# Performance work log

Hardware: AMD Instinct MI355X
Metric: run time of the kernel (lower is better)

The kernel has to match this reference:

```python
import jax, jax.numpy as jnp
import numpy as np

N_NODES = 100000
N_EDGES = 1600000
N_PAIRS = 200000
IN_C, HID_C, OUT_C = 128, 128, 64


def setup_inputs() -> dict:
    key = jax.random.key(0)
    ks = jax.random.split(key, 10)
    x = jax.random.normal(ks[0], (N_NODES, IN_C), dtype=jnp.float32)
    edge_index = jax.random.randint(ks[1], (2, N_EDGES), 0, N_NODES, dtype=jnp.int64)
    node_i = jax.random.randint(ks[2], (N_PAIRS,), 0, N_NODES, dtype=jnp.int64)
    node_j = jax.random.randint(ks[3], (N_PAIRS,), 0, N_NODES, dtype=jnp.int64)
    def glorot(k, fan_in, fan_out):
        s = jnp.sqrt(6.0 / (fan_in + fan_out))
        return jax.random.uniform(k, (fan_in, fan_out), jnp.float32, -s, s)
    W1 = glorot(ks[4], IN_C, HID_C)
    b1 = jnp.zeros((HID_C,), jnp.float32)
    W2 = glorot(ks[5], HID_C, HID_C)
    b2 = jnp.zeros((HID_C,), jnp.float32)
    W3 = glorot(ks[6], HID_C, OUT_C)
    b3 = jnp.zeros((OUT_C,), jnp.float32)
    return {"x": x, "edge_index": edge_index, "node_i": node_i, "node_j": node_j,
            "W1": W1, "b1": b1, "W2": W2, "b2": b2, "W3": W3, "b3": b3}


def _gcn_layer(h, src, dst, deg_inv, w_e, W, b):
    # h: [N, Cin] -> linear then symmetric-normalized aggregation (with self loops)
    h = h @ W  # [N, Cout]
    msg = h[src] * w_e[:, None]  # [E, Cout] gather + edge weight
    agg = jax.ops.segment_sum(msg, dst, num_segments=N_NODES)
    agg = agg + h * deg_inv[:, None]  # self-loop term: h_i / deg_i
    return agg + b


def reference(x, edge_index, node_i, node_j, W1, b1, W2, b2, W3, b3):
    src, dst = edge_index[0], edge_index[1]
    # GCN normalization with self loops: deg_i = 1 + in-degree
    ones = jnp.ones((N_EDGES,), jnp.float32)
    deg = jax.ops.segment_sum(ones, dst, num_segments=N_NODES) + 1.0
    dinv_sqrt = jax.lax.rsqrt(deg)
    deg_inv = 1.0 / deg
    w_e = dinv_sqrt[src] * dinv_sqrt[dst]  # [E]

    h = _gcn_layer(x, src, dst, deg_inv, w_e, W1, b1)
    h = jax.nn.relu(h)  # dropout is identity in eval mode
    h = _gcn_layer(h, src, dst, deg_inv, w_e, W2, b2)
    h = jax.nn.relu(h)
    h = _gcn_layer(h, src, dst, deg_inv, w_e, W3, b3)

    # dot-product link decode (decode_type=None)
    return jnp.sum(h[node_i] * h[node_j], axis=-1)  # [N_PAIRS]
```

## Files before the change

kernel.cpp:

```cpp
#include <hip/hip_runtime.h>

#define NN 100000
#define NNP 100032
#define NE 1600000
#define NP 200000
#define NBKT 782
#define BCAP 3072
#define BKB 4096

typedef short s16x8 __attribute__((ext_vector_type(8)));
typedef float f32x4 __attribute__((ext_vector_type(4)));
typedef float f32x2 __attribute__((ext_vector_type(2)));

__device__ __forceinline__ unsigned short f2bf(float f) {
  unsigned int u = __float_as_uint(f);
  u += 0x7fffu + ((u >> 16) & 1u);
  return (unsigned short)(u >> 16);
}

__device__ __forceinline__ void pkadd(f32x2& a, uint u) {
  f32x2 v;
  v.x = __uint_as_float(u << 16);
  v.y = __uint_as_float(u & 0xffff0000u);
  asm("v_pk_add_f32 %0, %0, %1" : "+v"(a) : "v"(v));
}

__device__ __forceinline__ void rowadd(uint4 v, f32x2* a) {
  pkadd(a[0], v.x);
  pkadd(a[1], v.y);
  pkadd(a[2], v.z);
  pkadd(a[3], v.w);
}

template <int RSH>
__device__ __forceinline__ void gath(const int* __restrict__ col,
                                     const char* __restrict__ Tb, int s,
                                     int tend, uint co, f32x2* acc) {
  const int d = tend - s;
  const int nfull = d >> 3;
  const int rem = d & 7;
  int e = s;
  int c[8];
#pragma unroll
  for (int j = 0; j < 8; ++j) c[j] = col[e + j];
#pragma unroll 1
  for (int it = 0; it < nfull; ++it) {
    uint4 v0 = *(const uint4*)(Tb + (((uint)c[0] << RSH) | co));
    uint4 v1 = *(const uint4*)(Tb + (((uint)c[1] << RSH) | co));
    uint4 v2 = *(const uint4*)(Tb + (((uint)c[2] << RSH) | co));
    uint4 v3 = *(const uint4*)(Tb + (((uint)c[3] << RSH) | co));
    uint4 v4 = *(const uint4*)(Tb + (((uint)c[4] << RSH) | co));
    uint4 v5 = *(const uint4*)(Tb + (((uint)c[5] << RSH) | co));
    uint4 v6 = *(const uint4*)(Tb + (((uint)c[6] << RSH) | co));
    uint4 v7 = *(const uint4*)(Tb + (((uint)c[7] << RSH) | co));
    e += 8;
#pragma unroll
    for (int j = 0; j < 8; ++j) c[j] = col[e + j];
    rowadd(v0, acc);
    rowadd(v1, acc);
    rowadd(v2, acc);
    rowadd(v3, acc);
    rowadd(v4, acc);
    rowadd(v5, acc);
    rowadd(v6, acc);
    rowadd(v7, acc);
  }
  if (rem) {
#pragma unroll
    for (int j = 0; j < 8; ++j) c[j] = (j < rem) ? c[j] : NN;
    uint4 v0 = *(const uint4*)(Tb + (((uint)c[0] << RSH) | co));
    uint4 v1 = *(const uint4*)(Tb + (((uint)c[1] << RSH) | co));
    uint4 v2 = *(const uint4*)(Tb + (((uint)c[2] << RSH) | co));
    uint4 v3 = *(const uint4*)(Tb + (((uint)c[3] << RSH) | co));
    uint4 v4 = *(const uint4*)(Tb + (((uint)c[4] << RSH) | co));
    uint4 v5 = *(const uint4*)(Tb + (((uint)c[5] << RSH) | co));
    uint4 v6 = *(const uint4*)(Tb + (((uint)c[6] << RSH) | co));
    uint4 v7 = *(const uint4*)(Tb + (((uint)c[7] << RSH) | co));
    rowadd(v0, acc);
    rowadd(v1, acc);
    rowadd(v2, acc);
    rowadd(v3, acc);
    rowadd(v4, acc);
    rowadd(v5, acc);
    rowadd(v6, acc);
    rowadd(v7, acc);
  }
}

template <int NT>
__device__ __forceinline__ void prepw_dev(const float* __restrict__ W,
                                          uint* __restrict__ Wt, int tid) {
  constexpr int COUT = NT * 16;
  if (tid >= 4 * NT * 64) return;
  int lane = tid & 63, comb = tid >> 6;
  int ks = comb / NT, tl = comb % NT;
  int q = lane >> 4, n = lane & 15;
  uint w[4];
#pragma unroll
  for (int jj = 0; jj < 4; ++jj) {
    int k0 = ks * 32 + q * 8 + 2 * jj;
    uint lo = f2bf(W[k0 * COUT + tl * 16 + n]);
    uint hi = f2bf(W[(k0 + 1) * COUT + tl * 16 + n]);
    w[jj] = lo | (hi << 16);
  }
  ((uint4*)Wt)[comb * 64 + lane] = make_uint4(w[0], w[1], w[2], w[3]);
}

__global__ __launch_bounds__(256) void k_setup(const float* __restrict__ W1,
                                               const float* __restrict__ W2,
                                               const float* __restrict__ W3,
                                               uint* __restrict__ Wt1,
                                               uint* __restrict__ Wt2,
                                               uint* __restrict__ Wt3,
                                               int* __restrict__ gcur) {
  int b = blockIdx.x, t = threadIdx.x;
  if (b < 4) {
    int i = b * 256 + t;
    if (i < 1024) gcur[i] = 0;
  } else if (b < 12) {
    prepw_dev<8>(W1, Wt1, (b - 4) * 256 + t);
  } else if (b < 20) {
    prepw_dev<8>(W2, Wt2, (b - 12) * 256 + t);
  } else {
    prepw_dev<4>(W3, Wt3, (b - 20) * 256 + t);
  }
}

__global__ __launch_bounds__(256) void k_bucket(const int* __restrict__ ei,
                                                int* __restrict__ gcur,
                                                int* __restrict__ aux) {
  __shared__ int cnt[1024];
  __shared__ int scn[1024];
  __shared__ int cur[1024];
  __shared__ int sc[256];
  __shared__ int sorted[BKB];
  __shared__ unsigned short sbkt[BKB];
  const int t = threadIdx.x;
  const int base = blockIdx.x * BKB;

  for (int i = t; i < 1024; i += 256) cnt[i] = 0;
  __syncthreads();

  int pk[16], bk[16];
#pragma unroll
  for (int i = 0; i < 16; ++i) {
    int e = base + t + 256 * i;
    if (e < NE) {
      int src = ei[e], dst = ei[NE + e];
      bk[i] = dst >> 7;
      pk[i] = src | ((dst & 127) << 17);
      atomicAdd(&cnt[bk[i]], 1);
    } else {
      bk[i] = -1;
    }
  }
  __syncthreads();

  int s0 = cnt[4 * t], s1 = cnt[4 * t + 1], s2 = cnt[4 * t + 2], s3 = cnt[4 * t + 3];
  int local = s0 + s1 + s2 + s3;
  sc[t] = local;
  __syncthreads();
  for (int off = 1; off < 256; off <<= 1) {
    int a = (t >= off) ? sc[t - off] : 0;
    __syncthreads();
    sc[t] += a;
    __syncthreads();
  }
  int b0 = sc[t] - local;
  scn[4 * t] = b0;
  scn[4 * t + 1] = b0 + s0;
  scn[4 * t + 2] = b0 + s0 + s1;
  scn[4 * t + 3] = b0 + s0 + s1 + s2;
  cur[4 * t] = scn[4 * t];
  cur[4 * t + 1] = scn[4 * t + 1];
  cur[4 * t + 2] = scn[4 * t + 2];
  cur[4 * t + 3] = scn[4 * t + 3];
  __syncthreads();
  const int tot = sc[255];

#pragma unroll
  for (int i = 0; i < 16; ++i) {
    if (bk[i] >= 0) {
      int pos = atomicAdd(&cur[bk[i]], 1);
      sorted[pos] = pk[i];
      sbkt[pos] = (unsigned short)bk[i];
    }
  }
  __syncthreads();

  for (int b = t; b < 1024; b += 256) {
    int c = cnt[b];
    if (c > 0) cur[b] = b * BCAP + atomicAdd(&gcur[b], c);
  }
  __syncthreads();

  for (int k = t; k < tot; k += 256) {
    int b = sbkt[k];
    aux[cur[b] + (k - scn[b])] = sorted[k];
  }
}

__global__ __launch_bounds__(256) void k_csr(const int* __restrict__ gcur,
                                             const int* __restrict__ aux,
                                             int* __restrict__ row_ptr,
                                             float* __restrict__ dinv,
                                             int* __restrict__ col) {
  __shared__ int red[256];
  __shared__ int c[128];
  __shared__ int cur[128];
  const int b = blockIdx.x, t = threadIdx.x;
  int p = 0;
  for (int i = t; i < b; i += 256) p += gcur[i];
  red[t] = p;
  if (t < 128) c[t] = 0;
  __syncthreads();
  for (int off = 128; off > 0; off >>= 1) {
    if (t < off) red[t] += red[t + off];
    __syncthreads();
  }
  const int base = red[0];
  const int m = gcur[b];
  const int* a = aux + (size_t)b * BCAP;
  __syncthreads();
  for (int k = t; k < m; k += 256) atomicAdd(&c[a[k] >> 17], 1);
  __syncthreads();
  int val = (t < 128) ? c[t] : 0;
  red[t] = val;
  __syncthreads();
  for (int off = 1; off < 128; off <<= 1) {
    int add = (t >= off && t < 128) ? red[t - off] : 0;
    __syncthreads();
    if (t < 128) red[t] += add;
    __syncthreads();
  }
  if (t < 128) {
    int excl = red[t] - val + base;
    int node = b * 128 + t;
    if (node < NN) {
      row_ptr[node] = excl;
      dinv[node] = rsqrtf((float)(val + 1));
      cur[t] = excl;
    }
  }
  if (b == NBKT - 1 && t == 0) row_ptr[NN] = base + m;
  __syncthreads();
  for (int k = t; k < m; k += 256) {
    int pk2 = a[k];
    int pos = atomicAdd(&cur[pk2 >> 17], 1);
    col[pos] = pk2 & 0x1FFFF;
  }
}

__global__ __launch_bounds__(256) void k_gemm1(const float* __restrict__ A,
                                               const uint* __restrict__ Wt,
                                               const float* __restrict__ dinv,
                                               unsigned short* __restrict__ T) {
  constexpr int NT = 8, COUT = 128;
  __shared__ __align__(16) uint Wlds[4 * NT * 64 * 4];
  __shared__ __align__(16) unsigned short Obuf[64 * COUT];
  const int t = threadIdx.x;
  {
    const uint4* src = (const uint4*)Wt;
    uint4* dst = (uint4*)Wlds;
    for (int i = t; i < 4 * NT * 64; i += 256) dst[i] = src[i];
  }
  __syncthreads();

  const int wv = t >> 6, lane = t & 63;
  const int n = lane & 15, quad = lane >> 4;
  const int rbase = blockIdx.x * 64 + wv * 16;

  union AB { uint4 u; s16x8 s; };
  AB a[4];
  {
    int row = rbase + n;
    if (row >= NN) row = NN - 1;
    const float* ap = A + (size_t)row * 128;
#pragma unroll
    for (int ks = 0; ks < 4; ++ks) {
      float4 v0 = *(const float4*)(ap + ks * 32 + quad * 8);
      float4 v1 = *(const float4*)(ap + ks * 32 + quad * 8 + 4);
      a[ks].u.x = (uint)f2bf(v0.x) | ((uint)f2bf(v0.y) << 16);
      a[ks].u.y = (uint)f2bf(v0.z) | ((uint)f2bf(v0.w) << 16);
      a[ks].u.z = (uint)f2bf(v1.x) | ((uint)f2bf(v1.y) << 16);
      a[ks].u.w = (uint)f2bf(v1.z) | ((uint)f2bf(v1.w) << 16);
    }
  }

  f32x4 acc[NT];
#pragma unroll
  for (int tl = 0; tl < NT; ++tl) acc[tl] = (f32x4){0.f, 0.f, 0.f, 0.f};

#pragma unroll
  for (int ks = 0; ks < 4; ++ks) {
#pragma unroll
    for (int tl = 0; tl < NT; ++tl) {
      AB b;
      b.u = *(const uint4*)&Wlds[((ks * NT + tl) * 64 + lane) * 4];
      acc[tl] = __builtin_amdgcn_mfma_f32_16x16x32_bf16(a[ks].s, b.s, acc[tl], 0, 0, 0);
    }
  }

  float4 dv = *(const float4*)(dinv + rbase + quad * 4);
  float dvv[4] = {dv.x, dv.y, dv.z, dv.w};
  unsigned short* ob = Obuf + wv * 16 * COUT;
#pragma unroll
  for (int tl = 0; tl < NT; ++tl)
#pragma unroll
    for (int r = 0; r < 4; ++r)
      ob[(quad * 4 + r) * COUT + tl * 16 + n] = f2bf(acc[tl][r] * dvv[r]);

  uint4* gdst = (uint4*)(T + (size_t)rbase * COUT);
#pragma unroll
  for (int i = 0; i < 4; ++i) {
    int off16 = i * 64 + lane;
    int lrow = (off16 * 8) / COUT;
    uint4 v = make_uint4(0u, 0u, 0u, 0u);
    if (rbase + lrow < NN) v = *(const uint4*)&ob[off16 * 8];
    gdst[off16] = v;
  }
}

template <int COUT>
__global__ __launch_bounds__(256) void k_gg(const int* __restrict__ row_ptr,
                                            const int* __restrict__ col,
                                            const uint4* __restrict__ T4,
                                            const float* __restrict__ dinv,
                                            const float* __restrict__ bias,
                                            const uint4* __restrict__ Wt,
                                            unsigned short* __restrict__ Tout) {
  constexpr int NT = COUT / 16;
  constexpr int TLW = NT / 4;
  constexpr int OSTR = COUT + 8;
  __shared__ __align__(16) uint4 Alds[16 * 17];
  const int t = threadIdx.x, wv = t >> 6, lane = t & 63;
  const int nbase = blockIdx.x * 16;
  const int q = lane >> 4, cl = lane & 15;

  const int node = nbase + wv * 4 + q;
  int s = 0, tend = 0;
  if (node < NN) {
    s = row_ptr[node];
    tend = row_ptr[node + 1];
  }
  const char* Tb = (const char*)T4;
  const uint co = (uint)cl << 4;
  f32x2 acc[4];
  acc[0] = (f32x2){0.f, 0.f};
  acc[1] = (f32x2){0.f, 0.f};
  acc[2] = (f32x2){0.f, 0.f};
  acc[3] = (f32x2){0.f, 0.f};
  rowadd(*(const uint4*)(Tb + (((uint)node << 8) | co)), acc);
  gath<8>(col, Tb, s, tend, co, acc);

  {
    float dv = dinv[node];
    float4 b0 = *(const float4*)&bias[cl * 8];
    float4 b1 = *(const float4*)&bias[cl * 8 + 4];
    float r0 = fmaxf(fmaf(dv, acc[0].x, b0.x), 0.f);
    float r1 = fmaxf(fmaf(dv, acc[0].y, b0.y), 0.f);
    float r2 = fmaxf(fmaf(dv, acc[1].x, b0.z), 0.f);
    float r3 = fmaxf(fmaf(dv, acc[1].y, b0.w), 0.f);
    float r4 = fmaxf(fmaf(dv, acc[2].x, b1.x), 0.f);
    float r5 = fmaxf(fmaf(dv, acc[2].y, b1.y), 0.f);
    float r6 = fmaxf(fmaf(dv, acc[3].x, b1.z), 0.f);
    float r7 = fmaxf(fmaf(dv, acc[3].y, b1.w), 0.f);
    uint4 o;
    o.x = (uint)f2bf(r0) | ((uint)f2bf(r1) << 16);
    o.y = (uint)f2bf(r2) | ((uint)f2bf(r3) << 16);
    o.z = (uint)f2bf(r4) | ((uint)f2bf(r5) << 16);
    o.w = (uint)f2bf(r6) | ((uint)f2bf(r7) << 16);
    Alds[(wv * 4 + q) * 17 + cl] = o;
  }
  __syncthreads();

  const int n = lane & 15, quad = lane >> 4;
  union AB { uint4 u; s16x8 s; };
  AB a[4];
#pragma unroll
  for (int ks = 0; ks < 4; ++ks) a[ks].u = Alds[n * 17 + ks * 4 + quad];
  f32x4 acc2[TLW];
#pragma unroll
  for (int j = 0; j < TLW; ++j) acc2[j] = (f32x4){0.f, 0.f, 0.f, 0.f};
#pragma unroll
  for (int ks = 0; ks < 4; ++ks) {
#pragma unroll
    for (int j = 0; j < TLW; ++j) {
      int tl = wv * TLW + j;
      AB b;
      b.u = Wt[(ks * NT + tl) * 64 + lane];
      acc2[j] = __builtin_amdgcn_mfma_f32_16x16x32_bf16(a[ks].s, b.s, acc2[j], 0, 0, 0);
    }
  }
  __syncthreads();

  unsigned short* Obuf = (unsigned short*)Alds;
  float4 dv4 = *(const float4*)(dinv + nbase + quad * 4);
  float dvv[4] = {dv4.x, dv4.y, dv4.z, dv4.w};
#pragma unroll
  for (int j = 0; j < TLW; ++j) {
    int tl = wv * TLW + j;
#pragma unroll
    for (int r = 0; r < 4; ++r)
      Obuf[(quad * 4 + r) * OSTR + tl * 16 + n] = f2bf(acc2[j][r] * dvv[r]);
  }
  __syncthreads();

  if constexpr (COUT == 128) {
    int row = t >> 4, c16 = t & 15;
    uint4 v = make_uint4(0u, 0u, 0u, 0u);
    if (nbase + row < NN) v = *(const uint4*)&Obuf[row * OSTR + c16 * 8];
    ((uint4*)(Tout + (size_t)nbase * COUT))[row * 16 + c16] = v;
  } else {
    if (t < 128) {
      int row = t >> 3, c16 = t & 7;
      uint4 v = make_uint4(0u, 0u, 0u, 0u);
      if (nbase + row < NN) v = *(const uint4*)&Obuf[row * OSTR + c16 * 8];
      ((uint4*)(Tout + (size_t)nbase * COUT))[row * 8 + c16] = v;
    }
  }
}

__global__ __launch_bounds__(256) void k_gather3(const int* __restrict__ row_ptr,
                                                 const int* __restrict__ col,
                                                 const uint4* __restrict__ T4,
                                                 uint4* __restrict__ G3) {
  const int wid = (blockIdx.x * 256 + threadIdx.x) >> 6;
  const int lane = threadIdx.x & 63;
  const int g = lane >> 3, cl = lane & 7;
  const int node = wid * 8 + g;
  if (node >= NN) return;
  int s = row_ptr[node], tend = row_ptr[node + 1];
  const char* Tb = (const char*)T4;
  const uint co = (uint)cl << 4;
  f32x2 acc[4];
  acc[0] = (f32x2){0.f, 0.f};
  acc[1] = (f32x2){0.f, 0.f};
  acc[2] = (f32x2){0.f, 0.f};
  acc[3] = (f32x2){0.f, 0.f};
  rowadd(*(const uint4*)(Tb + (((uint)node << 7) | co)), acc);
  gath<7>(col, Tb, s, tend, co, acc);
  uint4 o;
  o.x = (uint)f2bf(acc[0].x) | ((uint)f2bf(acc[0].y) << 16);
  o.y = (uint)f2bf(acc[1].x) | ((uint)f2bf(acc[1].y) << 16);
  o.z = (uint)f2bf(acc[2].x) | ((uint)f2bf(acc[2].y) << 16);
  o.w = (uint)f2bf(acc[3].x) | ((uint)f2bf(acc[3].y) << 16);
  G3[(size_t)node * 8 + cl] = o;
}

__global__ __launch_bounds__(256) void k_decode(const int* __restrict__ ni,
                                                const int* __restrict__ nj,
                                                const uint2* __restrict__ G3,
                                                const float* __restrict__ dinv,
                                                const float* __restrict__ b3,
                                                float* __restrict__ out) {
  int p = blockIdx.x * 16 + (threadIdx.x >> 4);
  int cl = threadIdx.x & 15;
  int i = ni[p], j = nj[p];
  uint2 ui = G3[(size_t)i * 16 + cl];
  uint2 uj = G3[(size_t)j * 16 + cl];
  float4 bb = *(const float4*)&b3[cl * 4];
  float di = dinv[i], dj = dinv[j];
  float gi0 = __uint_as_float(ui.x << 16), gi1 = __uint_as_float(ui.x & 0xffff0000u);
  float gi2 = __uint_as_float(ui.y << 16), gi3 = __uint_as_float(ui.y & 0xffff0000u);
  float gj0 = __uint_as_float(uj.x << 16), gj1 = __uint_as_float(uj.x & 0xffff0000u);
  float gj2 = __uint_as_float(uj.y << 16), gj3 = __uint_as_float(uj.y & 0xffff0000u);
  float v = fmaf(di, gi0, bb.x) * fmaf(dj, gj0, bb.x) +
            fmaf(di, gi1, bb.y) * fmaf(dj, gj1, bb.y) +
            fmaf(di, gi2, bb.z) * fmaf(dj, gj2, bb.z) +
            fmaf(di, gi3, bb.w) * fmaf(dj, gj3, bb.w);
  v += __shfl_xor(v, 1, 64);
  v += __shfl_xor(v, 2, 64);
  v += __shfl_xor(v, 4, 64);
  v += __shfl_xor(v, 8, 64);
  if (cl == 0) out[p] = v;
}

extern "C" void kernel_launch(void* const* d_in, const int* in_sizes, int n_in,
                              void* d_out, int out_size, void* d_ws, size_t ws_size,
                              hipStream_t stream) {
  const float* x  = (const float*)d_in[0];
  const int*   ei = (const int*)d_in[1];
  const int*   ni = (const int*)d_in[2];
  const int*   nj = (const int*)d_in[3];
  const float* W1 = (const float*)d_in[4];
  const float* b1 = (const float*)d_in[5];
  const float* W2 = (const float*)d_in[6];
  const float* b2 = (const float*)d_in[7];
  const float* W3 = (const float*)d_in[8];
  const float* b3 = (const float*)d_in[9];
  float* out = (float*)d_out;

  float* dinv    = (float*)d_ws;
  int*   row_ptr = (int*)(dinv + 102400);
  int*   gcur    = row_ptr + 102400;
  int*   col     = gcur + 1024;
  uint*  Wt1     = (uint*)(col + NE);
  uint*  Wt2     = Wt1 + 8192;
  uint*  Wt3     = Wt2 + 8192;
  uint*  Tbf     = Wt3 + 4096;
  uint*  T2      = Tbf + (size_t)NNP * 64;
  uint*  G3      = T2 + (size_t)NNP * 64;
  int*   aux     = (int*)G3;

  k_setup<<<24, 256, 0, stream>>>(W1, W2, W3, Wt1, Wt2, Wt3, gcur);
  k_bucket<<<(NE + BKB - 1) / BKB, 256, 0, stream>>>(ei, gcur, aux);
  k_csr<<<NBKT, 256, 0, stream>>>(gcur, aux, row_ptr, dinv, col);

  const int GB = NNP / 64;
  const int FB = NNP / 16;
  const int GATB = NN / 32;

  k_gemm1<<<GB, 256, 0, stream>>>(x, Wt1, dinv, (unsigned short*)Tbf);
  k_gg<128><<<FB, 256, 0, stream>>>(row_ptr, col, (const uint4*)Tbf, dinv, b1,
                                    (const uint4*)Wt2, (unsigned short*)T2);
  k_gg<64><<<FB, 256, 0, stream>>>(row_ptr, col, (const uint4*)T2, dinv, b2,
                                   (const uint4*)Wt3, (unsigned short*)Tbf);
  k_gather3<<<GATB, 256, 0, stream>>>(row_ptr, col, (const uint4*)Tbf, (uint4*)G3);
  k_decode<<<NP / 16, 256, 0, stream>>>(ni, nj, (const uint2*)G3, dinv, b3, out);
}
```

Baseline: 305.5 us.

## Enlarge gather-GEMM blocks, fold bias/scale into gather3, use nontemporal accesses

The fused gather+GEMM kernels now process 32 nodes per 512-thread block, so each block runs two 16-row MFMA tiles. The final layer's dinv scaling and bias move from the decode kernel into k_gather3, which also switches to 1024-thread blocks, leaving decode as a plain dot product. Column-index loads and the 128-wide output stores use nontemporal hints to reduce cache pollution. Storing biased bf16 values slightly changes rounding, and larger blocks may lower occupancy.

```diff
diff --git a/kernel.cpp b/kernel.cpp
--- a/kernel.cpp
+++ b/kernel.cpp
@@ -11,6 +11,7 @@
 typedef short s16x8 __attribute__((ext_vector_type(8)));
 typedef float f32x4 __attribute__((ext_vector_type(4)));
 typedef float f32x2 __attribute__((ext_vector_type(2)));
+typedef uint u32x4 __attribute__((ext_vector_type(4)));
 
 __device__ __forceinline__ unsigned short f2bf(float f) {
   unsigned int u = __float_as_uint(f);
@@ -30,6 +31,12 @@
   pkadd(a[1], v.y);
   pkadd(a[2], v.z);
   pkadd(a[3], v.w);
+}
+
+__device__ __forceinline__ void ntstore16(void* p, uint4 o) {
+  u32x4 v;
+  v.x = o.x; v.y = o.y; v.z = o.z; v.w = o.w;
+  __builtin_nontemporal_store(v, (u32x4*)p);
 }
 
 template <int RSH>
@@ -42,7 +49,7 @@
   int e = s;
   int c[8];
 #pragma unroll
-  for (int j = 0; j < 8; ++j) c[j] = col[e + j];
+  for (int j = 0; j < 8; ++j) c[j] = __builtin_nontemporal_load(&col[e + j]);
 #pragma unroll 1
   for (int it = 0; it < nfull; ++it) {
     uint4 v0 = *(const uint4*)(Tb + (((uint)c[0] << RSH) | co));
@@ -55,7 +62,7 @@
     uint4 v7 = *(const uint4*)(Tb + (((uint)c[7] << RSH) | co));
     e += 8;
 #pragma unroll
-    for (int j = 0; j < 8; ++j) c[j] = col[e + j];
+    for (int j = 0; j < 8; ++j) c[j] = __builtin_nontemporal_load(&col[e + j]);
     rowadd(v0, acc);
     rowadd(v1, acc);
     rowadd(v2, acc);
@@ -322,7 +329,7 @@
 }
 
 template <int COUT>
-__global__ __launch_bounds__(256) void k_gg(const int* __restrict__ row_ptr,
+__global__ __launch_bounds__(512) void k_gg(const int* __restrict__ row_ptr,
                                             const int* __restrict__ col,
                                             const uint4* __restrict__ T4,
                                             const float* __restrict__ dinv,
@@ -332,9 +339,9 @@
   constexpr int NT = COUT / 16;
   constexpr int TLW = NT / 4;
   constexpr int OSTR = COUT + 8;
-  __shared__ __align__(16) uint4 Alds[16 * 17];
+  __shared__ __align__(16) uint4 Alds[32 * 17];
   const int t = threadIdx.x, wv = t >> 6, lane = t & 63;
-  const int nbase = blockIdx.x * 16;
+  const int nbase = blockIdx.x * 32;
   const int q = lane >> 4, cl = lane & 15;
 
   const int node = nbase + wv * 4 + q;
@@ -375,10 +382,11 @@
   __syncthreads();
 
   const int n = lane & 15, quad = lane >> 4;
+  const int rt = wv >> 2;
   union AB { uint4 u; s16x8 s; };
   AB a[4];
 #pragma unroll
-  for (int ks = 0; ks < 4; ++ks) a[ks].u = Alds[n * 17 + ks * 4 + quad];
+  for (int ks = 0; ks < 4; ++ks) a[ks].u = Alds[(rt * 16 + n) * 17 + ks * 4 + quad];
   f32x4 acc2[TLW];
 #pragma unroll
   for (int j = 0; j < TLW; ++j) acc2[j] = (f32x4){0.f, 0.f, 0.f, 0.f};
@@ -386,7 +394,7 @@
   for (int ks = 0; ks < 4; ++ks) {
 #pragma unroll
     for (int j = 0; j < TLW; ++j) {
-      int tl = wv * TLW + j;
+      int tl = (wv & 3) * TLW + j;
       AB b;
       b.u = Wt[(ks * NT + tl) * 64 + lane];
       acc2[j] = __builtin_amdgcn_mfma_f32_16x16x32_bf16(a[ks].s, b.s, acc2[j], 0, 0, 0);
@@ -395,14 +403,14 @@
   __syncthreads();
 
   unsigned short* Obuf = (unsigned short*)Alds;
-  float4 dv4 = *(const float4*)(dinv + nbase + quad * 4);
+  float4 dv4 = *(const float4*)(dinv + nbase + rt * 16 + quad * 4);
   float dvv[4] = {dv4.x, dv4.y, dv4.z, dv4.w};
 #pragma unroll
   for (int j = 0; j < TLW; ++j) {
-    int tl = wv * TLW + j;
+    int tl = (wv & 3) * TLW + j;
 #pragma unroll
     for (int r = 0; r < 4; ++r)
-      Obuf[(quad * 4 + r) * OSTR + tl * 16 + n] = f2bf(acc2[j][r] * dvv[r]);
+      Obuf[(rt * 16 + quad * 4 + r) * OSTR + tl * 16 + n] = f2bf(acc2[j][r] * dvv[r]);
   }
   __syncthreads();
 
@@ -410,9 +418,9 @@
     int row = t >> 4, c16 = t & 15;
     uint4 v = make_uint4(0u, 0u, 0u, 0u);
     if (nbase + row < NN) v = *(const uint4*)&Obuf[row * OSTR + c16 * 8];
-    ((uint4*)(Tout + (size_t)nbase * COUT))[row * 16 + c16] = v;
+    ntstore16(&((uint4*)(Tout + (size_t)nbase * COUT))[row * 16 + c16], v);
   } else {
-    if (t < 128) {
+    if (t < 256) {
       int row = t >> 3, c16 = t & 7;
       uint4 v = make_uint4(0u, 0u, 0u, 0u);
       if (nbase + row < NN) v = *(const uint4*)&Obuf[row * OSTR + c16 * 8];
@@ -421,11 +429,13 @@
   }
 }
 
-__global__ __launch_bounds__(256) void k_gather3(const int* __restrict__ row_ptr,
-                                                 const int* __restrict__ col,
-                                                 const uint4* __restrict__ T4,
-                                                 uint4* __restrict__ G3) {
-  const int wid = (blockIdx.x * 256 + threadIdx.x) >> 6;
+__global__ __launch_bounds__(1024) void k_gather3(const int* __restrict__ row_ptr,
+                                                  const int* __restrict__ col,
+                                                  const uint4* __restrict__ T4,
+                                                  const float* __restrict__ dinv,
+                                                  const float* __restrict__ b3,
+                                                  uint4* __restrict__ G3) {
+  const int wid = (blockIdx.x * 1024 + threadIdx.x) >> 6;
   const int lane = threadIdx.x & 63;
   const int g = lane >> 3, cl = lane & 7;
   const int node = wid * 8 + g;
@@ -440,35 +450,39 @@
   acc[3] = (f32x2){0.f, 0.f};
   rowadd(*(const uint4*)(Tb + (((uint)node << 7) | co)), acc);
   gath<7>(col, Tb, s, tend, co, acc);
+  float dv = dinv[node];
+  float4 bb0 = *(const float4*)&b3[cl * 8];
+  float4 bb1 = *(const float4*)&b3[cl * 8 + 4];
+  float h0 = fmaf(dv, acc[0].x, bb0.x);
+  float h1 = fmaf(dv, acc[0].y, bb0.y);
+  float h2 = fmaf(dv, acc[1].x, bb0.z);
+  float h3 = fmaf(dv, acc[1].y, bb0.w);
+  float h4 = fmaf(dv, acc[2].x, bb1.x);
+  float h5 = fmaf(dv, acc[2].y, bb1.y);
+  float h6 = fmaf(dv, acc[3].x, bb1.z);
+  float h7 = fmaf(dv, acc[3].y, bb1.w);
   uint4 o;
-  o.x = (uint)f2bf(acc[0].x) | ((uint)f2bf(acc[0].y) << 16);
-  o.y = (uint)f2bf(acc[1].x) | ((uint)f2bf(acc[1].y) << 16);
-  o.z = (uint)f2bf(acc[2].x) | ((uint)f2bf(acc[2].y) << 16);
-  o.w = (uint)f2bf(acc[3].x) | ((uint)f2bf(acc[3].y) << 16);
+  o.x = (uint)f2bf(h0) | ((uint)f2bf(h1) << 16);
+  o.y = (uint)f2bf(h2) | ((uint)f2bf(h3) << 16);
+  o.z = (uint)f2bf(h4) | ((uint)f2bf(h5) << 16);
+  o.w = (uint)f2bf(h6) | ((uint)f2bf(h7) << 16);
   G3[(size_t)node * 8 + cl] = o;
 }
 
 __global__ __launch_bounds__(256) void k_decode(const int* __restrict__ ni,
                                                 const int* __restrict__ nj,
                                                 const uint2* __restrict__ G3,
-                                                const float* __restrict__ dinv,
-                                                const float* __restrict__ b3,
                                                 float* __restrict__ out) {
   int p = blockIdx.x * 16 + (threadIdx.x >> 4);
   int cl = threadIdx.x & 15;
   int i = ni[p], j = nj[p];
   uint2 ui = G3[(size_t)i * 16 + cl];
   uint2 uj = G3[(size_t)j * 16 + cl];
-  float4 bb = *(const float4*)&b3[cl * 4];
-  float di = dinv[i], dj = dinv[j];
   float gi0 = __uint_as_float(ui.x << 16), gi1 = __uint_as_float(ui.x & 0xffff0000u);
   float gi2 = __uint_as_float(ui.y << 16), gi3 = __uint_as_float(ui.y & 0xffff0000u);
   float gj0 = __uint_as_float(uj.x << 16), gj1 = __uint_as_float(uj.x & 0xffff0000u);
   float gj2 = __uint_as_float(uj.y << 16), gj3 = __uint_as_float(uj.y & 0xffff0000u);
-  float v = fmaf(di, gi0, bb.x) * fmaf(dj, gj0, bb.x) +
-            fmaf(di, gi1, bb.y) * fmaf(dj, gj1, bb.y) +
-            fmaf(di, gi2, bb.z) * fmaf(dj, gj2, bb.z) +
-            fmaf(di, gi3, bb.w) * fmaf(dj, gj3, bb.w);
+  float v = gi0 * gj0 + gi1 * gj1 + gi2 * gj2 + gi3 * gj3;
   v += __shfl_xor(v, 1, 64);
   v += __shfl_xor(v, 2, 64);
   v += __shfl_xor(v, 4, 64);
@@ -508,14 +522,15 @@
   k_csr<<<NBKT, 256, 0, stream>>>(gcur, aux, row_ptr, dinv, col);
 
   const int GB = NNP / 64;
-  const int FB = NNP / 16;
-  const int GATB = NN / 32;
+  const int FB = NNP / 32;
+  const int GATB = (NN + 127) / 128;
 
   k_gemm1<<<GB, 256, 0, stream>>>(x, Wt1, dinv, (unsigned short*)Tbf);
-  k_gg<128><<<FB, 256, 0, stream>>>(row_ptr, col, (const uint4*)Tbf, dinv, b1,
+  k_gg<128><<<FB, 512, 0, stream>>>(row_ptr, col, (const uint4*)Tbf, dinv, b1,
                                     (const uint4*)Wt2, (unsigned short*)T2);
-  k_gg<64><<<FB, 256, 0, stream>>>(row_ptr, col, (const uint4*)T2, dinv, b2,
+  k_gg<64><<<FB, 512, 0, stream>>>(row_ptr, col, (const uint4*)T2, dinv, b2,
                                    (const uint4*)Wt3, (unsigned short*)Tbf);
-  k_gather3<<<GATB, 256, 0, stream>>>(row_ptr, col, (const uint4*)Tbf, (uint4*)G3);
-  k_decode<<<NP / 16, 256, 0, stream>>>(ni, nj, (const uint2*)G3, dinv, b3, out);
-}
+  k_gather3<<<GATB, 1024, 0, stream>>>(row_ptr, col, (const uint4*)Tbf, dinv, b3,
+                                       (uint4*)G3);
+  k_decode<<<NP / 16, 256, 0, stream>>>(ni, nj, (const uint2*)G3, out);
+}
```

Measured after the change: 321.3 us. +5.2%, slower.
